# Performance work log

Measured on AMD Instinct MI355X. Metric: run time of the kernel, lower is better.

## Reference

```python
import jax, jax.numpy as jnp
import numpy as np

B, C, H, W = 32, 128, 56, 56
CMAX, OUT, KS, K = 128, 256, 3, 4
HID = 64  # attn_fc hidden width


def setup_inputs() -> dict:
    key = jax.random.key(0)
    ks = jax.random.split(key, 6)
    x = jax.random.normal(ks[0], (B, C, H, W), dtype=jnp.float32)
    weight_bank = jax.random.normal(ks[1], (K, OUT, CMAX, KS, KS), dtype=jnp.float32)
    fc1_w = jax.random.normal(ks[2], (HID, CMAX), dtype=jnp.float32) * (1.0 / np.sqrt(CMAX))
    fc1_b = jnp.zeros((HID,), dtype=jnp.float32)
    fc2_w = jax.random.normal(ks[3], (K, HID), dtype=jnp.float32) * (1.0 / np.sqrt(HID))
    fc2_b = jnp.zeros((K,), dtype=jnp.float32)
    return {"x": x, "weight_bank": weight_bank, "fc1_w": fc1_w, "fc1_b": fc1_b,
            "fc2_w": fc2_w, "fc2_b": fc2_b}


def reference(x, weight_bank, fc1_w, fc1_b, fc2_w, fc2_b):
    b, c, h, w = x.shape
    # AdaptiveAvgPool2d(1) on zero-channel-padded input -> mean over HW, pad channel dim
    pooled = jnp.mean(x, axis=(2, 3))                       # [B, C]
    pooled = jnp.pad(pooled, ((0, 0), (0, CMAX - c)))       # [B, CMAX]
    hdn = jax.nn.relu(pooled @ fc1_w.T + fc1_b)             # [B, 64]
    attn = jax.nn.softmax(hdn @ fc2_w.T + fc2_b, axis=-1)   # [B, K]
    # per-sample kernel synthesis
    weight = jnp.einsum('bk,kocij->bocij', attn, weight_bank[:, :, :c])  # [B,O,C,k,k]
    # single grouped conv instead of B separate conv launches
    lhs = x.reshape(1, b * c, h, w)
    rhs = weight.reshape(b * OUT, c, KS, KS)
    p = KS // 2
    out = jax.lax.conv_general_dilated(
        lhs, rhs, window_strides=(1, 1), padding=[(p, p), (p, p)],
        feature_group_count=b,
        dimension_numbers=('NCHW', 'OIHW', 'NCHW'))
    return out.reshape(b, OUT, h, w)
```

## Files before the change

### kernel.cpp

```cpp
#include <hip/hip_runtime.h>
#include <hip/hip_bf16.h>

#define B_    32
#define C_    128
#define H_    56
#define W_    56
#define OUT_  256
#define K_    4
#define HID_  64
#define HW_   (H_*W_)
#define KV_   (C_*9)
#define PH_   58
#define PW_   58
#define PP_   (PH_*PW_)

typedef __attribute__((ext_vector_type(8))) short short8_t;
typedef __attribute__((ext_vector_type(4))) float float4_t;

typedef __hip_bfloat16 bf16;

__device__ __forceinline__ short f2bf(float v) {
    union { bf16 h; short s; } u; u.h = __float2bfloat16(v); return u.s;
}

typedef __attribute__((address_space(1))) const unsigned int* gas_t;
typedef __attribute__((address_space(3))) unsigned int* las_t;

__device__ __forceinline__ void gl_lds16(const short* g, short* l) {
    __builtin_amdgcn_global_load_lds((gas_t)(const void*)g, (las_t)(void*)l, 16, 0, 0);
}

__global__ __launch_bounds__(256) void dc_pool(const float* __restrict__ x,
                                               float* __restrict__ pooled) {
    int bc = blockIdx.x;
    const float4_t* xp = (const float4_t*)(x + (size_t)bc * HW_);
    float s = 0.f;
    for (int j = threadIdx.x; j < HW_/4; j += 256) {
        float4_t v = xp[j];
        s += v[0] + v[1] + v[2] + v[3];
    }
    #pragma unroll
    for (int off = 32; off; off >>= 1) s += __shfl_down(s, off, 64);
    __shared__ float ps[4];
    if ((threadIdx.x & 63) == 0) ps[threadIdx.x >> 6] = s;
    __syncthreads();
    if (threadIdx.x == 0) pooled[bc] = ps[0] + ps[1] + ps[2] + ps[3];
}

__global__ __launch_bounds__(256) void dc_xt(const float* __restrict__ x,
                                             short* __restrict__ xTp) {
    int b = blockIdx.y, n0 = blockIdx.x * 128;
    __shared__ short t[C_][130];
    for (int i = threadIdx.x; i < C_*128; i += 256) {
        int c = i >> 7, nn = i & 127;
        int pp = n0 + nn;
        int py = pp / PW_, px = pp - py*PW_;
        bool valid = (pp < PP_) & (py >= 1) & (py <= H_) & (px >= 1) & (px <= W_);
        float v = valid ? x[((size_t)b*C_ + c)*HW_ + (py-1)*W_ + (px-1)] : 0.f;
        t[c][nn] = f2bf(v);
    }
    __syncthreads();
    typedef __attribute__((ext_vector_type(2))) unsigned int uint2_t;
    for (int i = threadIdx.x; i < 32*128; i += 256) {
        int nn = i >> 5, c4 = (i & 31) * 4;
        int pp = n0 + nn;
        if (pp < PP_) {
            union { unsigned short u[4]; uint2_t v; } pk;
            pk.u[0] = (unsigned short)t[c4  ][nn];
            pk.u[1] = (unsigned short)t[c4+1][nn];
            pk.u[2] = (unsigned short)t[c4+2][nn];
            pk.u[3] = (unsigned short)t[c4+3][nn];
            *(uint2_t*)&xTp[((size_t)b*PP_ + pp)*C_ + c4] = pk.v;
        }
    }
}

__global__ __launch_bounds__(64) void dc_attn(const float* __restrict__ pooled,
                                              const float* __restrict__ fc1w,
                                              const float* __restrict__ fc1b,
                                              const float* __restrict__ fc2w,
                                              const float* __restrict__ fc2b,
                                              float* __restrict__ attn) {
    int b = blockIdx.x, h = threadIdx.x;
    __shared__ float pl[C_];
    __shared__ float hdn[HID_];
    __shared__ float logit[K_];
    pl[h]      = pooled[b*C_ + h]      * (1.0f / HW_);
    pl[h + 64] = pooled[b*C_ + 64 + h] * (1.0f / HW_);
    __syncthreads();
    float s = fc1b[h];
    #pragma unroll 8
    for (int c = 0; c < C_; ++c) s += pl[c] * fc1w[h*C_ + c];
    hdn[h] = fmaxf(s, 0.f);
    __syncthreads();
    if (h < K_) {
        float t = fc2b[h];
        #pragma unroll 8
        for (int j = 0; j < HID_; ++j) t += hdn[j] * fc2w[h*HID_ + j];
        logit[h] = t;
    }
    __syncthreads();
    if (h == 0) {
        float m = fmaxf(fmaxf(logit[0], logit[1]), fmaxf(logit[2], logit[3]));
        float e0 = __expf(logit[0]-m), e1 = __expf(logit[1]-m);
        float e2 = __expf(logit[2]-m), e3 = __expf(logit[3]-m);
        float inv = 1.0f / (e0+e1+e2+e3);
        attn[b*K_+0]=e0*inv; attn[b*K_+1]=e1*inv;
        attn[b*K_+2]=e2*inv; attn[b*K_+3]=e3*inv;
    }
}

__global__ __launch_bounds__(256) void dc_wsynth(const float* __restrict__ bank,
                                                 const float* __restrict__ attn,
                                                 bf16* __restrict__ Ws) {
    int o = blockIdx.x;
    int b0 = blockIdx.y * 8;
    __shared__ float wb[4*KV_];
    for (int i = threadIdx.x; i < 4*KV_; i += 256) {
        int kk = i / KV_, r = i - kk*KV_;
        wb[i] = bank[((size_t)kk*OUT_ + o)*KV_ + r];
    }
    __syncthreads();
    for (int bi = 0; bi < 8; ++bi) {
        int b = b0 + bi;
        float a0 = attn[b*K_+0], a1 = attn[b*K_+1];
        float a2 = attn[b*K_+2], a3 = attn[b*K_+3];
        unsigned* dst = (unsigned*)&Ws[((size_t)b*OUT_ + o)*KV_];
        for (int ii = threadIdx.x; ii < KV_/2; ii += 256) {
            int i0 = 2*ii;
            int tap0 = i0 >> 7, c0 = i0 & 127;
            int i1 = i0 + 1;
            int tap1 = i1 >> 7, c1 = i1 & 127;
            float v0 = a0*wb[c0*9+tap0] + a1*wb[KV_+c0*9+tap0]
                     + a2*wb[2*KV_+c0*9+tap0] + a3*wb[3*KV_+c0*9+tap0];
            float v1 = a0*wb[c1*9+tap1] + a1*wb[KV_+c1*9+tap1]
                     + a2*wb[2*KV_+c1*9+tap1] + a3*wb[3*KV_+c1*9+tap1];
            union { unsigned short u[2]; unsigned v; } pk;
            pk.u[0] = (unsigned short)f2bf(v0);
            pk.u[1] = (unsigned short)f2bf(v1);
            dst[ii] = pk.v;
        }
    }
}

__global__ __launch_bounds__(256) void dc_gemm(const short* __restrict__ Ws,
                                               const short* __restrict__ xTp,
                                               float* __restrict__ out) {
    int orig = blockIdx.x;
    int swz  = (orig & 7) * 200 + (orig >> 3);
    const int bx  = swz % 25;
    const int byz = swz / 25;
    const int by  = byz & 1;
    const int b   = byz >> 1;

    const int m0 = by * 128;
    const int n0 = bx * 128;
    const int tid  = threadIdx.x;
    const int lane = tid & 63;
    const int wv   = tid >> 6;
    const int wm   = wv & 1, wn = wv >> 1;
    const int l16  = lane & 15, quad = lane >> 4;

    __shared__ short lA[2][4096];
    __shared__ short lB[2][4096];

    const short* aG[2];
    const short* bG[2];
    int tOff[2];
    #pragma unroll
    for (int j = 0; j < 2; ++j) {
        int t = 2*wv + j;
        int row = t*16 + l16;
        aG[j] = Ws + ((size_t)b*OUT_ + m0 + row)*KV_ + quad*8;
        int n = n0 + row;
        int idc = min(n, HW_ - 1);
        int y = idc / W_, xx2 = idc - y * W_;
        int pbc = (y + 1) * PW_ + (xx2 + 1);
        bG[j] = xTp + ((size_t)b*PP_ + pbc)*C_ + quad*8;
        tOff[j] = t * 512;
    }

    int nidx[4];
    #pragma unroll
    for (int ni = 0; ni < 4; ++ni)
        nidx[ni] = n0 + wn*64 + ni*16 + l16;

    float4_t acc[4][4];
    #pragma unroll
    for (int mi = 0; mi < 4; ++mi)
        #pragma unroll
        for (int ni = 0; ni < 4; ++ni)
            acc[mi][ni] = (float4_t){0.f, 0.f, 0.f, 0.f};

    auto stage = [&](int ss, int buf) {
        int tap = ss >> 2, kq2 = ss & 3;
        int ty = tap / 3, tx = tap - 3*ty;
        int doff = ((ty - 1) * PW_ + (tx - 1)) * C_;
        int ka = tap*128 + kq2*32;
        int cb = kq2*32;
        #pragma unroll
        for (int j = 0; j < 2; ++j) {
            gl_lds16(aG[j] + ka,        &lA[buf][tOff[j]]);
            gl_lds16(bG[j] + doff + cb, &lB[buf][tOff[j]]);
        }
    };

    auto compute = [&](int buf) {
        short8_t af[4], bfr[4];
        #pragma unroll
        for (int mi = 0; mi < 4; ++mi)
            af[mi] = *(const short8_t*)(&lA[buf][(wm*4+mi)*512 + lane*8]);
        #pragma unroll
        for (int ni = 0; ni < 4; ++ni)
            bfr[ni] = *(const short8_t*)(&lB[buf][(wn*4+ni)*512 + lane*8]);
        #pragma unroll
        for (int mi = 0; mi < 4; ++mi)
            #pragma unroll
            for (int ni = 0; ni < 4; ++ni)
                acc[mi][ni] = __builtin_amdgcn_mfma_f32_16x16x32_bf16(
                    af[mi], bfr[ni], acc[mi][ni], 0, 0, 0);
    };

    stage(0, 0);
    __syncthreads();
    for (int ss = 0; ss < 36; ++ss) {
        int buf = ss & 1;
        if (ss < 35) stage(ss + 1, buf ^ 1);
        compute(buf);
        __syncthreads();
    }

    const size_t obase = (size_t)b * OUT_ * HW_;
    #pragma unroll
    for (int mi = 0; mi < 4; ++mi) {
        int m = m0 + wm*64 + mi*16 + quad*4;
        #pragma unroll
        for (int ni = 0; ni < 4; ++ni) {
            int n = nidx[ni];
            if (n < HW_) {
                float* op = out + obase + (size_t)m * HW_ + n;
                #pragma unroll
                for (int r = 0; r < 4; ++r)
                    op[(size_t)r * HW_] = acc[mi][ni][r];
            }
        }
    }
}

extern "C" void kernel_launch(void* const* d_in, const int* in_sizes, int n_in,
                              void* d_out, int out_size, void* d_ws, size_t ws_size,
                              hipStream_t stream) {
    const float* x    = (const float*)d_in[0];
    const float* bank = (const float*)d_in[1];
    const float* fc1w = (const float*)d_in[2];
    const float* fc1b = (const float*)d_in[3];
    const float* fc2w = (const float*)d_in[4];
    const float* fc2b = (const float*)d_in[5];
    float* out = (float*)d_out;

    char* ws = (char*)d_ws;
    float* pooled = (float*)ws;
    float* attn   = (float*)(ws + 16*1024);
    bf16*  Ws     = (bf16*) (ws + 32*1024);
    short* xTp    = (short*)(ws + 32*1024 + 18874368);

    dc_pool  <<<B_*C_, 256, 0, stream>>>(x, pooled);
    dc_xt    <<<dim3(27, B_), 256, 0, stream>>>(x, xTp);
    dc_attn  <<<B_,     64, 0, stream>>>(pooled, fc1w, fc1b, fc2w, fc2b, attn);
    dc_wsynth<<<dim3(OUT_, 4), 256, 0, stream>>>(bank, attn, Ws);
    dc_gemm  <<<dim3(1600), 256, 0, stream>>>((const short*)Ws, xTp, out);
}
```

Before: 321.3 us.

## Keep two global-to-LDS stages in flight with partial vmcnt waits

The main conv-GEMM loop now issues two stages of async global-to-LDS loads ahead. Each step waits only until the older stage has landed (vmcnt(4)) rather than draining all loads with __syncthreads, so loads can overlap the MFMA compute of the current buffer. It also replaces the divide by 3 with a multiply-shift and simplifies the offset arithmetic. The risk is correctness: the waitcnt and barrier sequence is hand-written and depends on the exact number of outstanding load instructions.

```diff
diff --git a/kernel.cpp b/kernel.cpp
--- a/kernel.cpp
+++ b/kernel.cpp
@@ -163,6 +163,8 @@
 
     __shared__ short lA[2][4096];
     __shared__ short lB[2][4096];
+    short* lAf = &lA[0][0];
+    short* lBf = &lB[0][0];
 
     const short* aG[2];
     const short* bG[2];
@@ -193,26 +195,31 @@
             acc[mi][ni] = (float4_t){0.f, 0.f, 0.f, 0.f};
 
     auto stage = [&](int ss, int buf) {
-        int tap = ss >> 2, kq2 = ss & 3;
-        int ty = tap / 3, tx = tap - 3*ty;
+        int tap = ss >> 2;
+        int ty  = (tap * 11) >> 5;
+        int tx  = tap - 3 * ty;
         int doff = ((ty - 1) * PW_ + (tx - 1)) * C_;
-        int ka = tap*128 + kq2*32;
-        int cb = kq2*32;
+        int ka = ss * 32;
+        int cb = (ss & 3) * 32;
+        short* la = lAf + buf * 4096;
+        short* lb = lBf + buf * 4096;
         #pragma unroll
         for (int j = 0; j < 2; ++j) {
-            gl_lds16(aG[j] + ka,        &lA[buf][tOff[j]]);
-            gl_lds16(bG[j] + doff + cb, &lB[buf][tOff[j]]);
+            gl_lds16(aG[j] + ka,        la + tOff[j]);
+            gl_lds16(bG[j] + doff + cb, lb + tOff[j]);
         }
     };
 
     auto compute = [&](int buf) {
+        const short* la = lAf + buf * 4096;
+        const short* lb = lBf + buf * 4096;
         short8_t af[4], bfr[4];
         #pragma unroll
         for (int mi = 0; mi < 4; ++mi)
-            af[mi] = *(const short8_t*)(&lA[buf][(wm*4+mi)*512 + lane*8]);
+            af[mi] = *(const short8_t*)(la + (wm*4+mi)*512 + lane*8);
         #pragma unroll
         for (int ni = 0; ni < 4; ++ni)
-            bfr[ni] = *(const short8_t*)(&lB[buf][(wn*4+ni)*512 + lane*8]);
+            bfr[ni] = *(const short8_t*)(lb + (wn*4+ni)*512 + lane*8);
         #pragma unroll
         for (int mi = 0; mi < 4; ++mi)
             #pragma unroll
@@ -222,13 +229,20 @@
     };
 
     stage(0, 0);
-    __syncthreads();
-    for (int ss = 0; ss < 36; ++ss) {
+    stage(1, 1);
+    #pragma unroll 1
+    for (int ss = 0; ss < 35; ++ss) {
         int buf = ss & 1;
-        if (ss < 35) stage(ss + 1, buf ^ 1);
+        asm volatile("s_waitcnt vmcnt(4)" ::: "memory");
+        __builtin_amdgcn_s_barrier();
         compute(buf);
-        __syncthreads();
-    }
+        asm volatile("s_waitcnt lgkmcnt(0)" ::: "memory");
+        __builtin_amdgcn_s_barrier();
+        if (ss < 34) stage(ss + 2, buf);
+    }
+    asm volatile("s_waitcnt vmcnt(0)" ::: "memory");
+    __builtin_amdgcn_s_barrier();
+    compute(1);
 
     const size_t obase = (size_t)b * OUT_ * HW_;
     #pragma unroll
```

Result: no change. 320.4 us (-0.3%).

## Deepen GEMM LDS pipeline to four stages with explicit vmcnt waits

Applied to the files above, without the earlier changes.

The conv GEMM now keeps three tile loads in flight across a four-buffer LDS ring instead of double buffering. Manual `s_waitcnt vmcnt` plus a single `s_barrier` per iteration replace the two `__syncthreads` calls. The next stage is issued right after the LDS fragment reads, and MFMA issue priority is raised with `s_setprio`. The XCD-aware block swizzle is dropped in favour of a plain 3D grid, and tap/k index math is simplified. This doubles LDS use, which may lower occupancy, and the lost swizzle may reduce L2 locality across XCDs.

```diff
diff --git a/kernel.cpp b/kernel.cpp
--- a/kernel.cpp
+++ b/kernel.cpp
@@ -146,23 +146,17 @@
 __global__ __launch_bounds__(256) void dc_gemm(const short* __restrict__ Ws,
                                                const short* __restrict__ xTp,
                                                float* __restrict__ out) {
-    int orig = blockIdx.x;
-    int swz  = (orig & 7) * 200 + (orig >> 3);
-    const int bx  = swz % 25;
-    const int byz = swz / 25;
-    const int by  = byz & 1;
-    const int b   = byz >> 1;
-
-    const int m0 = by * 128;
-    const int n0 = bx * 128;
+    const int b  = blockIdx.z;
+    const int m0 = blockIdx.y * 128;
+    const int n0 = blockIdx.x * 128;
     const int tid  = threadIdx.x;
     const int lane = tid & 63;
     const int wv   = tid >> 6;
     const int wm   = wv & 1, wn = wv >> 1;
     const int l16  = lane & 15, quad = lane >> 4;
 
-    __shared__ short lA[2][4096];
-    __shared__ short lB[2][4096];
+    __shared__ short lA[4][4096];
+    __shared__ short lB[4][4096];
 
     const short* aG[2];
     const short* bG[2];
@@ -193,11 +187,12 @@
             acc[mi][ni] = (float4_t){0.f, 0.f, 0.f, 0.f};
 
     auto stage = [&](int ss, int buf) {
-        int tap = ss >> 2, kq2 = ss & 3;
-        int ty = tap / 3, tx = tap - 3*ty;
+        int tap = ss >> 2;
+        int ty  = (tap * 11) >> 5;
+        int tx  = tap - 3 * ty;
         int doff = ((ty - 1) * PW_ + (tx - 1)) * C_;
-        int ka = tap*128 + kq2*32;
-        int cb = kq2*32;
+        int ka = ss * 32;
+        int cb = (ss & 3) * 32;
         #pragma unroll
         for (int j = 0; j < 2; ++j) {
             gl_lds16(aG[j] + ka,        &lA[buf][tOff[j]]);
@@ -205,7 +200,18 @@
         }
     };
 
-    auto compute = [&](int buf) {
+    stage(0, 0);
+    stage(1, 1);
+    stage(2, 2);
+
+    #pragma unroll 1
+    for (int ss = 0; ss < 36; ++ss) {
+        const int buf = ss & 3;
+        if (ss < 34)       asm volatile("s_waitcnt vmcnt(8)" ::: "memory");
+        else if (ss == 34) asm volatile("s_waitcnt vmcnt(4)" ::: "memory");
+        else               asm volatile("s_waitcnt vmcnt(0)" ::: "memory");
+        __builtin_amdgcn_s_barrier();
+
         short8_t af[4], bfr[4];
         #pragma unroll
         for (int mi = 0; mi < 4; ++mi)
@@ -213,21 +219,17 @@
         #pragma unroll
         for (int ni = 0; ni < 4; ++ni)
             bfr[ni] = *(const short8_t*)(&lB[buf][(wn*4+ni)*512 + lane*8]);
+
+        if (ss + 3 < 36) stage(ss + 3, (ss + 3) & 3);
+
+        __builtin_amdgcn_s_setprio(1);
         #pragma unroll
         for (int mi = 0; mi < 4; ++mi)
             #pragma unroll
             for (int ni = 0; ni < 4; ++ni)
                 acc[mi][ni] = __builtin_amdgcn_mfma_f32_16x16x32_bf16(
                     af[mi], bfr[ni], acc[mi][ni], 0, 0, 0);
-    };
-
-    stage(0, 0);
-    __syncthreads();
-    for (int ss = 0; ss < 36; ++ss) {
-        int buf = ss & 1;
-        if (ss < 35) stage(ss + 1, buf ^ 1);
-        compute(buf);
-        __syncthreads();
+        __builtin_amdgcn_s_setprio(0);
     }
 
     const size_t obase = (size_t)b * OUT_ * HW_;
@@ -268,5 +270,5 @@
     dc_xt    <<<dim3(27, B_), 256, 0, stream>>>(x, xTp);
     dc_attn  <<<B_,     64, 0, stream>>>(pooled, fc1w, fc1b, fc2w, fc2b, attn);
     dc_wsynth<<<dim3(OUT_, 4), 256, 0, stream>>>(bank, attn, Ws);
-    dc_gemm  <<<dim3(1600), 256, 0, stream>>>((const short*)Ws, xTp, out);
-}
+    dc_gemm  <<<dim3(25, 2, B_), 256, 0, stream>>>((const short*)Ws, xTp, out);
+}
```

Measured after the change: 320.0 us. No clear change (-0.4%).
